# Kernel optimization log

Hardware: AMD Instinct MI355X
Metric: run time of the kernel (lower is better)

The kernel has to match this reference:

```python
import jax, jax.numpy as jnp
import numpy as np

D = 512      # d_model
H = 8        # n_head
NL = 3       # encoder layers
FF = 2048    # torch TransformerEncoderLayer default dim_feedforward
HID = 256    # hidden_size
ACT = 12     # action_size
NOBJ = 89    # num_objects
BAND = 17    # tril(diagonal=-17) -> keys older than 16 steps banned


def setup_inputs() -> dict:
    key = jax.random.key(0)
    ks = iter(jax.random.split(key, 48))
    rn = lambda shape, s=0.02: jax.random.normal(next(ks), shape, jnp.float32) * s
    b, seq = 16, 512
    inp = {
        'state_input': jax.random.normal(next(ks), (b, seq, 3, 16, 16), jnp.float32),
        'goal_input': jax.random.normal(next(ks), (b, seq, 300), jnp.float32),
        # encoders (stand-ins for obs_enc / lang_enc)
        'W_obs': rn((256, 3 * 16 * 16)), 'b_obs': rn((256,)),
        'W_lang': rn((256, 300)), 'b_lang': rn((256,)),
        # input projection 512 -> 512
        'W_in': rn((D, 512)), 'b_in': rn((D,)),
        # per-layer transformer params, stacked on layer dim
        'Wqkv': rn((NL, 3 * D, D)), 'bqkv': rn((NL, 3 * D)),
        'Wo': rn((NL, D, D)), 'bo': rn((NL, D)),
        'W1': rn((NL, FF, D)), 'b1': rn((NL, FF)),
        'W2': rn((NL, D, FF)), 'b2': rn((NL, D)),
        'g1': jnp.ones((NL, D)), 'bt1': jnp.zeros((NL, D)),
        'g2': jnp.ones((NL, D)), 'bt2': jnp.zeros((NL, D)),
        # output heads
        'W_outp': rn((HID, D)), 'b_outp': rn((HID,)),
        'W_a1': rn((ACT, HID)), 'b_a1': rn((ACT,)),
        'W_a2': rn((NOBJ, HID)), 'b_a2': rn((NOBJ,)),
    }
    return inp


def _ln(y, g, bt):
    m = y.mean(-1, keepdims=True)
    v = y.var(-1, keepdims=True)
    return (y - m) / jnp.sqrt(v + 1e-5) * g + bt


def _encoder(x, mask_add, Wqkv, bqkv, Wo, bo, W1, b1, W2, b2, g1, bt1, g2, bt2):
    b, n, _ = x.shape
    dh = D // H
    scale = 1.0 / np.sqrt(dh)
    for l in range(NL):
        qkv = x @ Wqkv[l].T + bqkv[l]
        q, k, v = jnp.split(qkv, 3, axis=-1)
        hd = lambda t: t.reshape(b, n, H, dh).transpose(0, 2, 1, 3)  # [b,h,n,dh]
        q, k, v = hd(q), hd(k), hd(v)
        sc = jnp.einsum('bhqd,bhkd->bhqk', q, k) * scale + mask_add
        a = jax.nn.softmax(sc, axis=-1)
        o = jnp.einsum('bhqk,bhkd->bhqd', a, v).transpose(0, 2, 1, 3).reshape(b, n, D)
        o = o @ Wo[l].T + bo[l]
        x = _ln(x + o, g1[l], bt1[l])             # post-LN (torch default)
        f = jax.nn.relu(x @ W1[l].T + b1[l]) @ W2[l].T + b2[l]
        x = _ln(x + f, g2[l], bt2[l])
    return x


def reference(state_input, goal_input, W_obs, b_obs, W_lang, b_lang, W_in, b_in,
              Wqkv, bqkv, Wo, bo, W1, b1, W2, b2, g1, bt1, g2, bt2,
              W_outp, b_outp, W_a1, b_a1, W_a2, b_a2):
    b, s = state_input.shape[:2]
    st = state_input.reshape(b, s, -1) @ W_obs.T + b_obs          # obs_enc
    lg = goal_input @ W_lang.T + b_lang                            # lang_enc
    x = jnp.concatenate([st, lg], axis=-1) @ W_in.T + b_in        # [b,s,D]
    # key padding mask; sentinel token appended (causal_mask=False branch)
    pad = ~jnp.any(goal_input != -1, axis=-1)                      # [b,s]
    pad = jnp.concatenate([pad, jnp.zeros((b, 1), bool)], axis=1)
    x = jnp.concatenate([x, jnp.zeros((b, 1, D), x.dtype)], axis=1)
    n = s + 1
    i = jnp.arange(n)
    # banned: tril(-17) | triu(1)  -> attend only to keys in [i-16, i]
    mask2 = ((i[:, None] - i[None, :]) >= BAND) | (i[None, :] > i[:, None])
    banned = mask2[None, None, :, :] | pad[:, None, None, :]
    mask_add = jnp.where(banned, jnp.float32(-1e9), jnp.float32(0.0))
    x = _encoder(x, mask_add, Wqkv, bqkv, Wo, bo, W1, b1, W2, b2, g1, bt1, g2, bt2)
    out = x[:, :-1, :]                                             # drop sentinel
    h = out @ W_outp.T + b_outp
    l1 = h @ W_a1.T + b_a1
    l2 = h @ W_a2.T + b_a2
    return jnp.concatenate([l1, l2], axis=-1)                      # [b,s,101]
```

## Files before the change

kernel.cpp:

```cpp
#include <hip/hip_runtime.h>

#define D 512
#define H 8
#define NL 3
#define FFD 2048
#define HID 256
#define BAND 17
#define BATCH 16
#define SEQ 512
#define MTOK (BATCH * SEQ)
#define NOUT 101
#define NOUTP 128

typedef unsigned short u16;
typedef __attribute__((ext_vector_type(8))) short short8;
typedef __attribute__((ext_vector_type(4))) float f32x4;
typedef __attribute__((ext_vector_type(8))) unsigned short u16x8;

__device__ inline float bf2f(u16 u) {
    union { unsigned int i; float f; } x; x.i = ((unsigned int)u) << 16; return x.f;
}
__device__ inline u16 f2bf(float f) {
    union { float f; unsigned int i; } x; x.f = f;
    unsigned int r = x.i + 0x7fffu + ((x.i >> 16) & 1u);
    return (u16)(r >> 16);
}

__device__ __forceinline__ void gload_lds16(const u16* g, u16* l) {
    __builtin_amdgcn_global_load_lds(
        (const __attribute__((address_space(1))) unsigned int*)(g),
        (__attribute__((address_space(3))) unsigned int*)(l),
        16, 0, 0);
}

#define BM 128
#define BN 128
#define BK 64

__global__ __launch_bounds__(512) void gemm_kernel(
    const u16* __restrict__ A, int lda,
    const u16* __restrict__ B, int ldb,
    const float* __restrict__ bias,
    float* __restrict__ Cf, int ldcf,
    u16* __restrict__ Cb0, u16* __restrict__ Cb1, int ldcb,
    int M, int N, int K, int relu)
{
    __shared__ u16 As[2][BM * BK];
    __shared__ u16 Bs[2][BN * BK];
    const int tid  = threadIdx.x;
    const int lane = tid & 63;
    const int wv   = tid >> 6;
    const int wr = wv >> 2, wc = wv & 3;

    const int nb  = gridDim.x * gridDim.y;
    const int bid = blockIdx.y * gridDim.x + blockIdx.x;
    const int tile = (bid & 7) * (nb >> 3) + (bid >> 3);
    const int m0 = (tile / gridDim.x) * BM;
    const int n0 = (tile % gridDim.x) * BN;
    const int kz = blockIdx.z * K;

    f32x4 acc[4][2] = {};

    const int srow8 = lane >> 3;
    const int schunk = (lane & 7) ^ srow8;
    const size_t aoff0 = (size_t)(m0 + wv * 16 + srow8) * lda + kz + schunk * 8;
    const size_t aoff1 = aoff0 + 8 * lda;
    const size_t boff0 = (size_t)(n0 + wv * 16 + srow8) * ldb + kz + schunk * 8;
    const size_t boff1 = boff0 + 8 * ldb;

    const int frow = lane & 15;
    const int q    = lane >> 4;
    const int rc0 = ((q ^ (frow & 7)) << 3);
    const int rc1 = (((4 + q) ^ (frow & 7)) << 3);

    #define STAGE(buf, k0)                                                    \
        do {                                                                  \
            gload_lds16(A + aoff0 + (k0), &As[buf][(wv * 16 + 0) * BK]);      \
            gload_lds16(A + aoff1 + (k0), &As[buf][(wv * 16 + 8) * BK]);      \
            gload_lds16(B + boff0 + (k0), &Bs[buf][(wv * 16 + 0) * BK]);      \
            gload_lds16(B + boff1 + (k0), &Bs[buf][(wv * 16 + 8) * BK]);      \
        } while (0)

    #define COMPUTE(buf)                                                            \
        do {                                                                        \
            short8 af[4][2], bf[2][2];                                              \
            _Pragma("unroll")                                                       \
            for (int i = 0; i < 4; ++i) {                                           \
                const u16* rp = &As[buf][(wr * 64 + i * 16 + frow) * BK];           \
                af[i][0] = *(const short8*)&rp[rc0];                                \
                af[i][1] = *(const short8*)&rp[rc1];                                \
            }                                                                       \
            _Pragma("unroll")                                                       \
            for (int j = 0; j < 2; ++j) {                                           \
                const u16* rp = &Bs[buf][(wc * 32 + j * 16 + frow) * BK];           \
                bf[j][0] = *(const short8*)&rp[rc0];                                \
                bf[j][1] = *(const short8*)&rp[rc1];                                \
            }                                                                       \
            _Pragma("unroll")                                                       \
            for (int kk = 0; kk < 2; ++kk)                                          \
                _Pragma("unroll")                                                   \
                for (int i = 0; i < 4; ++i)                                         \
                    _Pragma("unroll")                                               \
                    for (int j = 0; j < 2; ++j)                                     \
                        acc[i][j] = __builtin_amdgcn_mfma_f32_16x16x32_bf16(        \
                            af[i][kk], bf[j][kk], acc[i][j], 0, 0, 0);              \
        } while (0)

    const int nt = K >> 6;
    STAGE(0, 0);
    int cur = 0;
    for (int t = 0; t < nt - 1; ++t) {
        STAGE(cur ^ 1, (t + 1) << 6);
        asm volatile("s_waitcnt vmcnt(4)" ::: "memory");
        __builtin_amdgcn_s_barrier();
        __builtin_amdgcn_sched_barrier(0);
        COMPUTE(cur);
        __builtin_amdgcn_s_barrier();
        cur ^= 1;
    }
    asm volatile("s_waitcnt vmcnt(0)" ::: "memory");
    __builtin_amdgcn_s_barrier();
    __builtin_amdgcn_sched_barrier(0);
    COMPUTE(cur);

    #undef STAGE
    #undef COMPUTE

    u16* Cb = blockIdx.z ? Cb1 : Cb0;
    const bool addb = (bias != nullptr) && (blockIdx.z == 0);

    const int crow0 = (lane >> 4) * 4;
    const int ccol  = lane & 15;
    #pragma unroll
    for (int j = 0; j < 2; ++j) {
        int gcol = n0 + wc * 32 + j * 16 + ccol;
        if (gcol >= N) continue;
        float bv = addb ? bias[gcol] : 0.f;
        #pragma unroll
        for (int i = 0; i < 4; ++i) {
            #pragma unroll
            for (int r = 0; r < 4; ++r) {
                int grow = m0 + wr * 64 + i * 16 + crow0 + r;
                float v = acc[i][j][r] + bv;
                if (relu) v = fmaxf(v, 0.f);
                if (Cf) Cf[(size_t)grow * ldcf + gcol] = v;
                if (Cb) Cb[(size_t)grow * ldcb + gcol] = f2bf(v);
            }
        }
    }
}

#define CHUNK 128
#define KSLOT 144
#define VT_LD 152

__global__ __launch_bounds__(512) void attn_kernel(
    const u16* __restrict__ qkv, const unsigned char* __restrict__ pad,
    u16* __restrict__ o)
{
    __shared__ u16 Vt[64 * VT_LD];
    __shared__ u16 Pl[8 * 16 * 40];
    __shared__ unsigned char padl[KSLOT];

    const int tid = threadIdx.x, lane = tid & 63, wv = tid >> 6;
    const int b = blockIdx.z, h = blockIdx.y, c0 = blockIdx.x * CHUNK;
    const u16* base = qkv + (size_t)b * SEQ * (3 * D);

    for (int s = tid; s < KSLOT * 4; s += 512) {
        int t = s >> 2, dq = (s & 3) * 16;
        int j = c0 - 16 + t; if (j < 0) j = 0;
        const u16* vrow = base + (size_t)j * (3 * D) + 2 * D + h * 64 + dq;
        u16 tmp[16];
        *(u16x8*)&tmp[0] = *(const u16x8*)&vrow[0];
        *(u16x8*)&tmp[8] = *(const u16x8*)&vrow[8];
        #pragma unroll
        for (int d = 0; d < 16; ++d)
            Vt[(dq + d) * VT_LD + t] = tmp[d];
    }
    if (tid < KSLOT) {
        int j = c0 - 16 + tid;
        padl[tid] = (j >= 0) ? pad[b * SEQ + j] : (unsigned char)1;
    }
    __syncthreads();

    const int qi0 = wv * 16;
    const int i0  = c0 + qi0;
    const int frow = lane & 15;
    const int g    = lane >> 4;
    const int kg8  = g * 8;
    const int g4   = g * 4;

    short8 qf[2];
    #pragma unroll
    for (int kk = 0; kk < 2; ++kk)
        qf[kk] = *(const short8*)&base[(size_t)(i0 + frow) * (3 * D) + h * 64 + kk * 32 + kg8];

    f32x4 sacc[2] = {};
    #pragma unroll
    for (int jb = 0; jb < 2; ++jb) {
        int jrow = i0 - 16 + jb * 16 + frow; if (jrow < 0) jrow = 0;
        const u16* kbase = base + (size_t)jrow * (3 * D) + D + h * 64;
        #pragma unroll
        for (int kk = 0; kk < 2; ++kk) {
            short8 kf = *(const short8*)&kbase[kk * 32 + kg8];
            sacc[jb] = __builtin_amdgcn_mfma_f32_16x16x32_bf16(qf[kk], kf, sacc[jb], 0, 0, 0);
        }
    }

    float sv[2][4];
    #pragma unroll
    for (int jb = 0; jb < 2; ++jb) {
        int s = jb * 16 + frow;
        int jg = i0 - 16 + s;
        bool padk = (jg < 0) || padl[qi0 + s];
        #pragma unroll
        for (int r = 0; r < 4; ++r) {
            int qq = g4 + r;
            bool banned = (s < qq) || (s > qq + 16) || padk;
            sv[jb][r] = sacc[jb][r] * 0.125f + (banned ? -1e9f : 0.f);
        }
    }

    float ex[2][4], rdn[4];
    #pragma unroll
    for (int r = 0; r < 4; ++r) {
        float m = fmaxf(sv[0][r], sv[1][r]);
        #pragma unroll
        for (int off = 1; off < 16; off <<= 1) m = fmaxf(m, __shfl_xor(m, off));
        float e0 = __expf(sv[0][r] - m);
        float e1 = __expf(sv[1][r] - m);
        float dsum = e0 + e1;
        #pragma unroll
        for (int off = 1; off < 16; off <<= 1) dsum += __shfl_xor(dsum, off);
        ex[0][r] = e0; ex[1][r] = e1;
        rdn[r] = 1.f / dsum;
    }

    u16* Pw = &Pl[wv * 640];
    #pragma unroll
    for (int jb = 0; jb < 2; ++jb)
        #pragma unroll
        for (int r = 0; r < 4; ++r)
            Pw[(g4 + r) * 40 + jb * 16 + frow] = f2bf(ex[jb][r]);
    short8 pa = *(const short8*)&Pw[frow * 40 + kg8];

    f32x4 oacc[4] = {};
    #pragma unroll
    for (int nb = 0; nb < 4; ++nb) {
        short8 vf = *(const short8*)&Vt[(nb * 16 + frow) * VT_LD + qi0 + kg8];
        oacc[nb] = __builtin_amdgcn_mfma_f32_16x16x32_bf16(pa, vf, oacc[nb], 0, 0, 0);
    }

    #pragma unroll
    for (int r = 0; r < 4; ++r) {
        size_t row = (size_t)(b * SEQ + i0 + g4 + r);
        #pragma unroll
        for (int nb = 0; nb < 4; ++nb)
            o[row * D + h * 64 + nb * 16 + frow] = f2bf(oacc[nb][r] * rdn[r]);
    }
}

__global__ __launch_bounds__(256) void resln_kernel(
    const u16* __restrict__ xin,
    const u16* __restrict__ d0, const u16* __restrict__ d1,
    const float* __restrict__ g, const float* __restrict__ bt,
    u16* __restrict__ xb)
{
    int row  = blockIdx.x * 4 + (threadIdx.x >> 6);
    int lane = threadIdx.x & 63;
    u16x8 xv = *(const u16x8*)(xin + (size_t)row * D + lane * 8);
    u16x8 dv0 = *(const u16x8*)(d0 + (size_t)row * D + lane * 8);
    u16x8 dv1 = *(const u16x8*)(d1 + (size_t)row * D + lane * 8);

    float y[8];
    float s = 0.f, s2 = 0.f;
    #pragma unroll
    for (int c = 0; c < 8; ++c) {
        y[c] = bf2f(xv[c]) + bf2f(dv0[c]) + bf2f(dv1[c]);
        s += y[c]; s2 += y[c] * y[c];
    }
    #pragma unroll
    for (int off = 32; off > 0; off >>= 1) {
        s  += __shfl_xor(s, off);
        s2 += __shfl_xor(s2, off);
    }
    float mean = s * (1.f / D);
    float var  = s2 * (1.f / D) - mean * mean;
    float inv  = rsqrtf(fmaxf(var, 0.f) + 1e-5f);

    f32x4 gv0 = ((const f32x4*)g)[lane * 2],  gv1 = ((const f32x4*)g)[lane * 2 + 1];
    f32x4 bv0 = ((const f32x4*)bt)[lane * 2], bv1 = ((const f32x4*)bt)[lane * 2 + 1];
    u16x8 ob;
    #pragma unroll
    for (int c = 0; c < 4; ++c) {
        ob[c]     = f2bf((y[c] - mean) * inv * gv0[c] + bv0[c]);
        ob[c + 4] = f2bf((y[c + 4] - mean) * inv * gv1[c] + bv1[c]);
    }
    *(u16x8*)(xb + (size_t)row * D + lane * 8) = ob;
}

struct CvtJob { const float* src; u16* dstb; float* dstf; int n; int mode; };
struct CvtArgs { CvtJob j[16]; int blk0[17]; };

__global__ __launch_bounds__(256) void cvt_kernel(CvtArgs a) {
    const int bx = blockIdx.x;
    int jid = 0;
    #pragma unroll 1
    while (jid < 15 && bx >= a.blk0[jid + 1]) ++jid;
    const CvtJob jb = a.j[jid];

    if (jb.mode == 5) {
        int row  = (bx - a.blk0[jid]) * 4 + (threadIdx.x >> 6);
        int lane = threadIdx.x & 63;
        const f32x4* gr = (const f32x4*)(jb.src + (size_t)row * 300);
        bool any = false;
        for (int c4 = lane; c4 < 75; c4 += 64) {
            f32x4 v = gr[c4];
            any |= (v[0] != -1.f) | (v[1] != -1.f) | (v[2] != -1.f) | (v[3] != -1.f);
        }
        unsigned long long b = __ballot(any);
        if (lane == 0) ((unsigned char*)jb.dstb)[row] = (b == 0ull) ? 1 : 0;
        return;
    }

    const int i0 = (bx - a.blk0[jid]) * 2048 + threadIdx.x * 8;
    if (i0 >= jb.n) return;

    if (jb.mode == 0) {
        if (i0 + 8 <= jb.n) {
            f32x4 v0 = *(const f32x4*)(jb.src + i0);
            f32x4 v1 = *(const f32x4*)(jb.src + i0 + 4);
            u16x8 o;
            #pragma unroll
            for (int c = 0; c < 4; ++c) { o[c] = f2bf(v0[c]); o[c + 4] = f2bf(v1[c]); }
            *(u16x8*)(jb.dstb + i0) = o;
        } else {
            for (int e = 0; e < 8 && i0 + e < jb.n; ++e) jb.dstb[i0 + e] = f2bf(jb.src[i0 + e]);
        }
    } else if (jb.mode == 2) {
        int r = (int)((unsigned)i0 / 320u);
        int c = i0 - r * 320;
        const float* s = jb.src + (size_t)r * 300 + c;
        u16x8 o;
        if (c + 8 <= 300) {
            f32x4 v0 = *(const f32x4*)s;
            f32x4 v1 = *(const f32x4*)(s + 4);
            #pragma unroll
            for (int cc = 0; cc < 4; ++cc) { o[cc] = f2bf(v0[cc]); o[cc + 4] = f2bf(v1[cc]); }
        } else {
            #pragma unroll
            for (int e = 0; e < 8; ++e) o[e] = (c + e < 300) ? f2bf(s[e]) : (u16)0;
        }
        *(u16x8*)(jb.dstb + i0) = o;
    } else if (jb.mode == 1) {
        for (int e = 0; e < 8 && i0 + e < jb.n; ++e) jb.dstf[i0 + e] = jb.src[i0 + e];
    } else {
        u16x8 z = {0, 0, 0, 0, 0, 0, 0, 0};
        *(u16x8*)(jb.dstb + i0) = z;
    }
}


extern "C" void kernel_launch(void* const* d_in, const int* in_sizes, int n_in,
                              void* d_out, int out_size, void* d_ws, size_t ws_size,
                              hipStream_t stream)
{
    const float* state  = (const float*)d_in[0];
    const float* goal   = (const float*)d_in[1];
    const float* W_obs  = (const float*)d_in[2];
    const float* b_obs  = (const float*)d_in[3];
    const float* W_lang = (const float*)d_in[4];
    const float* b_lang = (const float*)d_in[5];
    const float* W_in   = (const float*)d_in[6];
    const float* b_in   = (const float*)d_in[7];
    const float* Wqkv   = (const float*)d_in[8];
    const float* bqkv   = (const float*)d_in[9];
    const float* Wo     = (const float*)d_in[10];
    const float* bo     = (const float*)d_in[11];
    const float* W1     = (const float*)d_in[12];
    const float* b1     = (const float*)d_in[13];
    const float* W2     = (const float*)d_in[14];
    const float* b2     = (const float*)d_in[15];
    const float* g1     = (const float*)d_in[16];
    const float* bt1    = (const float*)d_in[17];
    const float* g2     = (const float*)d_in[18];
    const float* bt2    = (const float*)d_in[19];
    const float* W_outp = (const float*)d_in[20];
    const float* b_outp = (const float*)d_in[21];
    const float* W_a1   = (const float*)d_in[22];
    const float* b_a1   = (const float*)d_in[23];
    const float* W_a2   = (const float*)d_in[24];
    const float* b_a2   = (const float*)d_in[25];

    char* ws = (char*)d_ws;
    size_t off = 0;
    auto alloc = [&](size_t bytes) -> void* {
        void* p = ws + off;
        off = (off + bytes + 255) & ~(size_t)255;
        return p;
    };

    u16* wqkv_b  = (u16*)alloc((size_t)NL * 1536 * D * 2);
    u16* wo_b    = (u16*)alloc((size_t)NL * D * D * 2);
    u16* w1_b    = (u16*)alloc((size_t)NL * FFD * D * 2);
    u16* w2_b    = (u16*)alloc((size_t)NL * D * FFD * 2);
    u16* wobs_b  = (u16*)alloc((size_t)256 * 768 * 2);
    u16* wlang_b = (u16*)alloc((size_t)256 * 320 * 2);
    u16* win_b   = (u16*)alloc((size_t)D * D * 2);
    u16* woutp_b = (u16*)alloc((size_t)HID * D * 2);
    u16* wa_b    = (u16*)alloc((size_t)NOUTP * HID * 2);
    float* ba_f  = (float*)alloc((size_t)NOUT * 4);
    u16* state_b = (u16*)alloc((size_t)MTOK * 768 * 2);
    u16* goal_b  = (u16*)alloc((size_t)MTOK * 320 * 2);
    u16* feat_b  = (u16*)alloc((size_t)MTOK * D * 2);
    u16* x_b     = (u16*)alloc((size_t)MTOK * D * 2);
    u16* qkv_b   = (u16*)alloc((size_t)MTOK * 3 * D * 2);
    u16* o_b     = (u16*)alloc((size_t)MTOK * D * 2);
    u16* delta_b = (u16*)alloc((size_t)MTOK * D * 2);
    u16* h1_b    = (u16*)alloc((size_t)MTOK * FFD * 2);
    u16* hout_b  = (u16*)alloc((size_t)MTOK * HID * 2);
    unsigned char* pad_u8 = (unsigned char*)alloc(MTOK);
    u16* delta2_b = state_b;
    (void)ws_size; (void)in_sizes; (void)n_in; (void)out_size;

    CvtArgs ca;
    int nj = 0, blks = 0;
    auto addj = [&](const float* s, u16* db, float* df, int n, int mode, int nblk) {
        ca.j[nj].src = s; ca.j[nj].dstb = db; ca.j[nj].dstf = df;
        ca.j[nj].n = n; ca.j[nj].mode = mode;
        ca.blk0[nj] = blks;
        blks += nblk;
        ++nj;
    };
    auto addf = [&](const float* s, u16* db, float* df, int n, int mode) {
        addj(s, db, df, n, mode, (n + 2047) / 2048);
    };
    addf(state,  state_b, nullptr, MTOK * 768, 0);
    addf(goal,   goal_b,  nullptr, MTOK * 320, 2);
    addf(Wqkv,   wqkv_b,  nullptr, NL * 1536 * D, 0);
    addf(Wo,     wo_b,    nullptr, NL * D * D, 0);
    addf(W1,     w1_b,    nullptr, NL * FFD * D, 0);
    addf(W2,     w2_b,    nullptr, NL * D * FFD, 0);
    addf(W_obs,  wobs_b,  nullptr, 256 * 768, 0);
    addf(W_lang, wlang_b, nullptr, 256 * 320, 2);
    addf(W_in,   win_b,   nullptr, D * D, 0);
    addf(W_outp, woutp_b, nullptr, HID * D, 0);
    addf(W_a1,   wa_b,            nullptr, 12 * HID, 0);
    addf(W_a2,   wa_b + 12 * HID, nullptr, 89 * HID, 0);
    addf(nullptr, wa_b + NOUT * HID, nullptr, (NOUTP - NOUT) * HID, 3);
    addf(b_a1,   nullptr, ba_f,      12, 1);
    addf(b_a2,   nullptr, ba_f + 12, 89, 1);
    addj(goal,   (u16*)pad_u8, nullptr, MTOK, 5, MTOK / 4);
    ca.blk0[nj] = blks;
    cvt_kernel<<<blks, 256, 0, stream>>>(ca);

    auto gemm = [&](const u16* A, int lda, const u16* B, int ldb, const float* bias,
                    float* Cf, int ldcf, u16* Cb0, u16* Cb1, int ldcb,
                    int N, int K, int relu, int ksplit) {
        dim3 grid((N + BN - 1) / BN, MTOK / BM, ksplit);
        gemm_kernel<<<grid, 512, 0, stream>>>(A, lda, B, ldb, bias, Cf, ldcf,
                                              Cb0, Cb1, ldcb, MTOK, N, K / ksplit, relu);
    };

    gemm(state_b, 768, wobs_b, 768, b_obs, nullptr, 0, feat_b, nullptr, D, 256, 768, 0, 1);
    gemm(goal_b, 320, wlang_b, 320, b_lang, nullptr, 0, feat_b + 256, nullptr, D, 256, 320, 0, 1);
    gemm(feat_b, D, win_b, D, b_in, nullptr, 0, x_b, nullptr, D, D, D, 0, 1);

    for (int l = 0; l < NL; ++l) {
        gemm(x_b, D, wqkv_b + (size_t)l * 1536 * D, D, bqkv + l * 1536,
             nullptr, 0, qkv_b, nullptr, 3 * D, 3 * D, D, 0, 1);
        {
            dim3 grid(SEQ / CHUNK, H, BATCH);
            attn_kernel<<<grid, 512, 0, stream>>>(qkv_b, pad_u8, o_b);
        }
        gemm(o_b, D, wo_b + (size_t)l * D * D, D, bo + l * D,
             nullptr, 0, delta_b, delta2_b, D, D, D, 0, 2);
        resln_kernel<<<MTOK / 4, 256, 0, stream>>>(x_b, delta_b, delta2_b,
                                                   g1 + l * D, bt1 + l * D, x_b);
        gemm(x_b, D, w1_b + (size_t)l * FFD * D, D, b1 + l * FFD,
             nullptr, 0, h1_b, nullptr, FFD, FFD, D, 1, 1);
        gemm(h1_b, FFD, w2_b + (size_t)l * D * FFD, FFD, b2 + l * D,
             nullptr, 0, delta_b, delta2_b, D, D, FFD, 0, 2);
        resln_kernel<<<MTOK / 4, 256, 0, stream>>>(x_b, delta_b, delta2_b,
                                                   g2 + l * D, bt2 + l * D, x_b);
    }

    gemm(x_b, D, woutp_b, D, b_outp, nullptr, 0, hout_b, nullptr, HID, HID, D, 0, 1);
    gemm(hout_b, HID, wa_b, HID, ba_f, (float*)d_out, NOUT, nullptr, nullptr, 0, NOUT, HID, 0, 1);
}
```

Baseline: 367.7 us.

## Halve GEMM K-tile and use triple-buffered LDS ring with one barrier

The GEMM k-step shrinks from 64 to 32, and LDS staging moves from a double buffer to a three-slot ring. This removes the second barrier per iteration, since the buffer being written is never the one being read. The swizzle pattern and load offsets are reworked for 32-wide rows. The trade is twice as many loop iterations, each with half the MFMA work, which adds loop and wait overhead and may overlap memory latency less well.

```diff
diff --git a/kernel.cpp b/kernel.cpp
--- a/kernel.cpp
+++ b/kernel.cpp
@@ -35,7 +35,7 @@
 
 #define BM 128
 #define BN 128
-#define BK 64
+#define BK 32
 
 __global__ __launch_bounds__(512) void gemm_kernel(
     const u16* __restrict__ A, int lda,
@@ -45,8 +45,8 @@
     u16* __restrict__ Cb0, u16* __restrict__ Cb1, int ldcb,
     int M, int N, int K, int relu)
 {
-    __shared__ u16 As[2][BM * BK];
-    __shared__ u16 Bs[2][BN * BK];
+    __shared__ u16 As[3][BM * BK];
+    __shared__ u16 Bs[3][BN * BK];
     const int tid  = threadIdx.x;
     const int lane = tid & 63;
     const int wv   = tid >> 6;
@@ -61,62 +61,48 @@
 
     f32x4 acc[4][2] = {};
 
-    const int srow8 = lane >> 3;
-    const int schunk = (lane & 7) ^ srow8;
-    const size_t aoff0 = (size_t)(m0 + wv * 16 + srow8) * lda + kz + schunk * 8;
-    const size_t aoff1 = aoff0 + 8 * lda;
-    const size_t boff0 = (size_t)(n0 + wv * 16 + srow8) * ldb + kz + schunk * 8;
-    const size_t boff1 = boff0 + 8 * ldb;
+    const int srow = lane >> 2;
+    const int schunk = (lane & 3) ^ ((srow >> 1) & 3);
+    const size_t aoff = (size_t)(m0 + wv * 16 + srow) * lda + kz + schunk * 8;
+    const size_t boff = (size_t)(n0 + wv * 16 + srow) * ldb + kz + schunk * 8;
 
     const int frow = lane & 15;
     const int q    = lane >> 4;
-    const int rc0 = ((q ^ (frow & 7)) << 3);
-    const int rc1 = (((4 + q) ^ (frow & 7)) << 3);
-
-    #define STAGE(buf, k0)                                                    \
-        do {                                                                  \
-            gload_lds16(A + aoff0 + (k0), &As[buf][(wv * 16 + 0) * BK]);      \
-            gload_lds16(A + aoff1 + (k0), &As[buf][(wv * 16 + 8) * BK]);      \
-            gload_lds16(B + boff0 + (k0), &Bs[buf][(wv * 16 + 0) * BK]);      \
-            gload_lds16(B + boff1 + (k0), &Bs[buf][(wv * 16 + 8) * BK]);      \
+    const int rcol = ((q ^ ((frow >> 1) & 3)) << 3);
+
+    #define STAGE(buf, k0)                                             \
+        do {                                                           \
+            gload_lds16(A + aoff + (k0), &As[buf][wv * 16 * BK]);      \
+            gload_lds16(B + boff + (k0), &Bs[buf][wv * 16 * BK]);      \
         } while (0)
 
     #define COMPUTE(buf)                                                            \
         do {                                                                        \
-            short8 af[4][2], bf[2][2];                                              \
+            short8 af[4], bf[2];                                                    \
             _Pragma("unroll")                                                       \
-            for (int i = 0; i < 4; ++i) {                                           \
-                const u16* rp = &As[buf][(wr * 64 + i * 16 + frow) * BK];           \
-                af[i][0] = *(const short8*)&rp[rc0];                                \
-                af[i][1] = *(const short8*)&rp[rc1];                                \
-            }                                                                       \
+            for (int i = 0; i < 4; ++i)                                             \
+                af[i] = *(const short8*)&As[buf][(wr * 64 + i * 16 + frow) * BK + rcol]; \
             _Pragma("unroll")                                                       \
-            for (int j = 0; j < 2; ++j) {                                           \
-                const u16* rp = &Bs[buf][(wc * 32 + j * 16 + frow) * BK];           \
-                bf[j][0] = *(const short8*)&rp[rc0];                                \
-                bf[j][1] = *(const short8*)&rp[rc1];                                \
-            }                                                                       \
+            for (int j = 0; j < 2; ++j)                                             \
+                bf[j] = *(const short8*)&Bs[buf][(wc * 32 + j * 16 + frow) * BK + rcol]; \
             _Pragma("unroll")                                                       \
-            for (int kk = 0; kk < 2; ++kk)                                          \
+            for (int i = 0; i < 4; ++i)                                             \
                 _Pragma("unroll")                                                   \
-                for (int i = 0; i < 4; ++i)                                         \
-                    _Pragma("unroll")                                               \
-                    for (int j = 0; j < 2; ++j)                                     \
-                        acc[i][j] = __builtin_amdgcn_mfma_f32_16x16x32_bf16(        \
-                            af[i][kk], bf[j][kk], acc[i][j], 0, 0, 0);              \
+                for (int j = 0; j < 2; ++j)                                         \
+                    acc[i][j] = __builtin_amdgcn_mfma_f32_16x16x32_bf16(            \
+                        af[i], bf[j], acc[i][j], 0, 0, 0);                          \
         } while (0)
 
-    const int nt = K >> 6;
+    const int nt = K >> 5;
     STAGE(0, 0);
-    int cur = 0;
+    int cur = 0, nxt = 1;
     for (int t = 0; t < nt - 1; ++t) {
-        STAGE(cur ^ 1, (t + 1) << 6);
-        asm volatile("s_waitcnt vmcnt(4)" ::: "memory");
+        STAGE(nxt, (t + 1) << 5);
+        asm volatile("s_waitcnt vmcnt(2)" ::: "memory");
         __builtin_amdgcn_s_barrier();
         __builtin_amdgcn_sched_barrier(0);
         COMPUTE(cur);
-        __builtin_amdgcn_s_barrier();
-        cur ^= 1;
+        cur = nxt; nxt = nxt + 1; if (nxt >= 3) nxt = 0;
     }
     asm volatile("s_waitcnt vmcnt(0)" ::: "memory");
     __builtin_amdgcn_s_barrier();
```

Result: slower. 390.9 us (+6.3%).
